# Kernel optimization log

Hardware: AMD Instinct MI355X
Metric: run time of the kernel (lower is better)

## Reference

```python
import jax, jax.numpy as jnp
import numpy as np

B, S, H = 2, 1024, 2048
NH, HD = 16, 128
L = 4  # num_prev_layers == attention_window


def _rope(x):
    # x: [..., S, D]; standard rotate-half RoPE, base 10000
    d = x.shape[-1]
    s = x.shape[-2]
    inv_freq = 1.0 / (10000.0 ** (jnp.arange(0, d, 2, dtype=jnp.float32) / d))
    freqs = jnp.outer(jnp.arange(s, dtype=jnp.float32), inv_freq)  # [S, d/2]
    cos, sin = jnp.cos(freqs), jnp.sin(freqs)
    x1, x2 = jnp.split(x, 2, axis=-1)
    return jnp.concatenate([x1 * cos - x2 * sin, x2 * cos + x1 * sin], axis=-1)


def setup_inputs() -> dict:
    key = jax.random.key(0)
    ks = jax.random.split(key, 8)
    std = 0.02
    return {
        "hidden_states": jax.random.normal(ks[0], (B, S, H), jnp.float32),
        "prev_hidden_states": jax.random.normal(ks[1], (L, B, S, H), jnp.float32),
        "Wq": jax.random.normal(ks[2], (H, NH * HD), jnp.float32) * std,
        "bq": jnp.zeros((NH * HD,), jnp.float32),
        "Wk": jax.random.normal(ks[3], (H, NH * HD), jnp.float32) * std,
        "bk": jnp.zeros((NH * HD,), jnp.float32),
        "Wv": jax.random.normal(ks[4], (H, NH * HD), jnp.float32) * std,
        "bv": jnp.zeros((NH * HD,), jnp.float32),
        "Wo": jax.random.normal(ks[5], (NH * HD, H), jnp.float32) * std,
        "bo": jnp.zeros((H,), jnp.float32),
        "Wg": jax.random.normal(ks[6], (H, L), jnp.float32) * std,
    }


def reference(hidden_states, prev_hidden_states, Wq, bq, Wk, bk, Wv, bv, Wo, bo, Wg):
    b, s, _ = hidden_states.shape
    # queries from current layer: [b, nh, s, hd], RoPE applied
    q = (hidden_states @ Wq + bq).reshape(b, s, NH, HD).transpose(0, 2, 1, 3)
    q = _rope(q)
    # keys/values from each prev layer: [L, b, nh, s, hd]
    k = (prev_hidden_states @ Wk + bk).reshape(L, b, s, NH, HD).transpose(0, 1, 3, 2, 4)
    k = _rope(k)
    v = (prev_hidden_states @ Wv + bv).reshape(L, b, s, NH, HD).transpose(0, 1, 3, 2, 4)
    # per-prev-layer attention (no mask)
    scores = jnp.einsum('bhqd,lbhkd->lbhqk', q, k) / jnp.sqrt(jnp.float32(HD))
    attn = jax.nn.softmax(scores, axis=-1)
    lo = jnp.einsum('lbhqk,lbhkd->lbhqd', attn, v)
    lo = lo.transpose(0, 1, 3, 2, 4).reshape(L, b, s, NH * HD)  # merge heads
    # softmax gate over pooled queries -> combine layer outputs
    layer_w = jax.nn.softmax(jnp.mean(hidden_states, axis=1) @ Wg, axis=-1)  # [b, L]
    out = jnp.einsum('lbsh,bl->bsh', lo, layer_w)
    return out @ Wo + bo
```

## Files before the change

### kernel.cpp

```cpp
#include <hip/hip_runtime.h>
#include <hip/hip_bf16.h>
#include <math.h>


typedef __bf16 bf16;
typedef __bf16 bf16x4v __attribute__((ext_vector_type(4)));
typedef __bf16 bf16x8 __attribute__((ext_vector_type(8)));
typedef float f32x4 __attribute__((ext_vector_type(4)));

#define DEV static __device__ __forceinline__

DEV void gload_lds16(const void* g, void* s) {
  __builtin_amdgcn_global_load_lds(
      (const __attribute__((address_space(1))) void*)g,
      (__attribute__((address_space(3))) void*)s, 16, 0, 0);
}

DEV f32x4 mfma16(bf16x8 a, bf16x8 b, f32x4 c) {
  return __builtin_amdgcn_mfma_f32_16x16x32_bf16(a, b, c, 0, 0, 0);
}

__global__ __launch_bounds__(256) void cvt_kernel(const float* __restrict__ in,
                                                  bf16* __restrict__ out, int n4) {
  int i = blockIdx.x * 256 + threadIdx.x;
  if (i >= n4) return;
  const float4 v = ((const float4*)in)[i];
  bf16x4v o;
  o.x = (bf16)v.x; o.y = (bf16)v.y; o.z = (bf16)v.z; o.w = (bf16)v.w;
  ((bf16x4v*)out)[i] = o;
}

__global__ __launch_bounds__(256) void twt_kernel(const float* __restrict__ W,
                                                  bf16* __restrict__ Wt) {
  __shared__ float tile[64][65];
  const int t = threadIdx.x;
  const int n0 = blockIdx.x * 64, k0 = blockIdx.y * 64;
#pragma unroll
  for (int ph = 0; ph < 16; ++ph) {
    int idx = ph * 256 + t, r = idx >> 6, c = idx & 63;
    tile[r][c] = W[(size_t)(k0 + r) * 2048 + n0 + c];
  }
  __syncthreads();
#pragma unroll
  for (int ph = 0; ph < 16; ++ph) {
    int idx = ph * 256 + t, r = idx >> 6, c = idx & 63;
    Wt[(size_t)(n0 + r) * 2048 + k0 + c] = (bf16)tile[c][r];
  }
}

__global__ __launch_bounds__(64) void rope_table_kernel(float* __restrict__ cosT,
                                                        float* __restrict__ sinT) {
  int s = blockIdx.x, j = threadIdx.x;
  float inv = powf(10000.0f, -(float)j * (1.0f / 64.0f));
  float a = (float)s * inv;
  cosT[s * 64 + j] = cosf(a);
  sinT[s * 64 + j] = sinf(a);
}

__global__ __launch_bounds__(256) void rope_kernel(const bf16* __restrict__ raw,
                                                   const float* __restrict__ cosT,
                                                   const float* __restrict__ sinT,
                                                   bf16* __restrict__ outp) {
  int rid = blockIdx.x * 16 + (threadIdx.x >> 4);
  int j = threadIdx.x & 15;
  int s = rid & 1023;
  const bf16* src = raw + (size_t)rid * 128 + 4 * j;
  bf16* dst = outp + (size_t)rid * 128 + 4 * j;
  bf16x4v x1 = *(const bf16x4v*)src;
  bf16x4v x2 = *(const bf16x4v*)(src + 64);
  f32x4 c = *(const f32x4*)(cosT + s * 64 + 4 * j);
  f32x4 sn = *(const f32x4*)(sinT + s * 64 + 4 * j);
  bf16x4v o1, o2;
#pragma unroll
  for (int k = 0; k < 4; ++k) {
    float a = (float)x1[k], b2 = (float)x2[k];
    o1[k] = (bf16)(a * c[k] - b2 * sn[k]);
    o2[k] = (bf16)(b2 * c[k] + a * sn[k]);
  }
  *(bf16x4v*)dst = o1;
  *(bf16x4v*)(dst + 64) = o2;
}

__global__ __launch_bounds__(256) void mean_part_kernel(const float* __restrict__ hs,
                                                        float* __restrict__ part) {
  int bc = blockIdx.x;
  int b = bc >> 3, c0 = (bc & 7) * 256;
  int ss = blockIdx.y;
  int col = c0 + threadIdx.x;
  float s = 0.f;
  for (int r = 0; r < 128; ++r)
    s += hs[((size_t)b * 1024 + ss * 128 + r) * 2048 + col];
  part[(size_t)ss * 4096 + b * 2048 + col] = s;
}

__global__ __launch_bounds__(256) void mean_fin_kernel(const float* __restrict__ part,
                                                       float* __restrict__ meanb) {
  int c = blockIdx.x * 256 + threadIdx.x;
  float s = 0.f;
#pragma unroll
  for (int j = 0; j < 8; ++j) s += part[(size_t)j * 4096 + c];
  meanb[c] = s * (1.0f / 1024.0f);
}

__global__ __launch_bounds__(256) void gate_kernel(const float* __restrict__ meanb,
                                                   const float* __restrict__ Wg,
                                                   float* __restrict__ lwout) {
  __shared__ float red[8][256];
  int t = threadIdx.x;
  float p[8];
#pragma unroll
  for (int j = 0; j < 8; ++j) p[j] = 0.f;
  for (int hh = t; hh < 2048; hh += 256) {
    float m0 = meanb[hh], m1 = meanb[2048 + hh];
#pragma unroll
    for (int ll = 0; ll < 4; ++ll) {
      float g = Wg[hh * 4 + ll];
      p[ll] += m0 * g;
      p[4 + ll] += m1 * g;
    }
  }
#pragma unroll
  for (int j = 0; j < 8; ++j) red[j][t] = p[j];
  __syncthreads();
  for (int s2 = 128; s2 > 0; s2 >>= 1) {
    if (t < s2) {
#pragma unroll
      for (int j = 0; j < 8; ++j) red[j][t] += red[j][t + s2];
    }
    __syncthreads();
  }
  if (t == 0) {
#pragma unroll
    for (int bb = 0; bb < 2; ++bb) {
      float v0 = red[bb * 4 + 0][0], v1 = red[bb * 4 + 1][0];
      float v2 = red[bb * 4 + 2][0], v3 = red[bb * 4 + 3][0];
      float mx = fmaxf(fmaxf(v0, v1), fmaxf(v2, v3));
      float e0 = __expf(v0 - mx), e1 = __expf(v1 - mx);
      float e2 = __expf(v2 - mx), e3 = __expf(v3 - mx);
      float inv = 1.0f / (e0 + e1 + e2 + e3);
      lwout[bb * 4 + 0] = e0 * inv;
      lwout[bb * 4 + 1] = e1 * inv;
      lwout[bb * 4 + 2] = e2 * inv;
      lwout[bb * 4 + 3] = e3 * inv;
    }
  }
}

template <int OUTMODE>
__global__ __launch_bounds__(256) void gemm_kernel(const bf16* __restrict__ A,
                                                   const bf16* __restrict__ Bt,
                                                   const float* __restrict__ bias,
                                                   void* __restrict__ Cout,
                                                   int M, int N, int K) {
  __shared__ __attribute__((aligned(16))) bf16 As[2][128 * 64];
  __shared__ __attribute__((aligned(16))) bf16 Bs[2][128 * 64];
  const int t = threadIdx.x;
  const int w = t >> 6, l = t & 63;
  const int lo = l & 15, hi = l >> 4;
  const int wr = w >> 1, wc = w & 1;

  const int nwg = gridDim.x * gridDim.y;
  int flat = blockIdx.y * gridDim.x + blockIdx.x;
  int swz = (flat & 7) * (nwg >> 3) + (flat >> 3);
  const int bx = swz % gridDim.x, by = swz / gridDim.x;

  f32x4 acc[4][4];
#pragma unroll
  for (int m = 0; m < 4; ++m)
#pragma unroll
    for (int n = 0; n < 4; ++n)
#pragma unroll
      for (int q = 0; q < 4; ++q) acc[m][n][q] = 0.f;

  int srow[4], scl[4];
#pragma unroll
  for (int p = 0; p < 4; ++p) {
    int id = p * 256 + t;
    int r = id >> 3, cph = id & 7;
    srow[p] = r;
    scl[p] = cph ^ (r & 7);
  }

  const bf16* Ab = A + (size_t)by * 128 * K;
  const bf16* Bb = Bt + (size_t)bx * 128 * K;

  auto stage = [&](int bi, int kt) {
#pragma unroll
    for (int p = 0; p < 4; ++p)
      gload_lds16(Ab + (size_t)srow[p] * K + kt + scl[p] * 8,
                  &As[bi][(p * 256 + w * 64) * 8]);
#pragma unroll
    for (int p = 0; p < 4; ++p)
      gload_lds16(Bb + (size_t)srow[p] * K + kt + scl[p] * 8,
                  &Bs[bi][(p * 256 + w * 64) * 8]);
  };

  stage(0, 0);
  int cur = 0;
  for (int kt = 0; kt < K; kt += 64) {
    if (kt + 64 < K) {
      stage(cur ^ 1, kt + 64);
      asm volatile("s_waitcnt vmcnt(8)" ::: "memory");
    } else {
      asm volatile("s_waitcnt vmcnt(0)" ::: "memory");
    }
    __builtin_amdgcn_s_barrier();
    __builtin_amdgcn_sched_barrier(0);
    __builtin_amdgcn_s_setprio(1);
#pragma unroll
    for (int ks = 0; ks < 2; ++ks) {
      bf16x8 af[4], bfr[4];
#pragma unroll
      for (int m = 0; m < 4; ++m) {
        int row = wr * 64 + m * 16 + lo;
        int ch = (ks * 4 + hi) ^ (row & 7);
        af[m] = *(const bf16x8*)&As[cur][row * 64 + ch * 8];
      }
#pragma unroll
      for (int n = 0; n < 4; ++n) {
        int row = wc * 64 + n * 16 + lo;
        int ch = (ks * 4 + hi) ^ (row & 7);
        bfr[n] = *(const bf16x8*)&Bs[cur][row * 64 + ch * 8];
      }
#pragma unroll
      for (int m = 0; m < 4; ++m)
#pragma unroll
        for (int n = 0; n < 4; ++n)
          acc[m][n] = mfma16(af[m], bfr[n], acc[m][n]);
    }
    __builtin_amdgcn_s_setprio(0);
    __builtin_amdgcn_s_barrier();
    cur ^= 1;
  }

#pragma unroll
  for (int n = 0; n < 4; ++n) {
    int col = bx * 128 + wc * 64 + n * 16 + lo;
    float bb = bias[col];
#pragma unroll
    for (int m = 0; m < 4; ++m) {
#pragma unroll
      for (int i = 0; i < 4; ++i) {
        size_t row = (size_t)by * 128 + wr * 64 + m * 16 + hi * 4 + i;
        float v = acc[m][n][i] + bb;
        if (OUTMODE == 1)
          ((float*)Cout)[row * N + col] = v;
        else if (OUTMODE == 0)
          ((bf16*)Cout)[row * N + col] = (bf16)v;
        else {
          size_t g = (row >> 10) * 16 + (col >> 7);
          ((bf16*)Cout)[(g * 1024 + (row & 1023)) * 128 + (col & 127)] = (bf16)v;
        }
      }
    }
  }
}

__global__ __launch_bounds__(512, 2) void gemm_kv_kernel(
    const bf16* __restrict__ prev, const bf16* __restrict__ WkT,
    const bf16* __restrict__ WvT, const float* __restrict__ bk,
    const float* __restrict__ bv, bf16* __restrict__ Kout,
    bf16* __restrict__ Vout) {
  __shared__ __attribute__((aligned(16))) bf16 As[2][16384];
  __shared__ __attribute__((aligned(16))) bf16 Bs[2][16384];
  const int t = threadIdx.x;
  const int w = t >> 6, l = t & 63;
  const int lo = l & 15, hi = l >> 4;
  const int wm = w >> 2, wn = w & 3;

  const int bid = blockIdx.x;
  const int grp = bid >> 8;
  const int sub = bid & 255;
  const int swz = (sub & 7) * 32 + (sub >> 3);
  const int mt = (grp == 0) ? (swz >> 3) : (swz & 7);
  const int nt = (grp == 0) ? (swz & 7) : (swz >> 3);
  const bf16* Ab = ((grp == 0) ? prev : WvT) + (size_t)mt * 256 * 2048;
  const bf16* Bb = ((grp == 0) ? WkT : prev) + (size_t)nt * 256 * 2048;

  const int r0 = t >> 2;
  const int c8 = ((t & 3) ^ ((r0 >> 1) & 3)) * 8;

  f32x4 acc[8][4];
#pragma unroll
  for (int m = 0; m < 8; ++m)
#pragma unroll
    for (int n = 0; n < 4; ++n)
#pragma unroll
      for (int q = 0; q < 4; ++q) acc[m][n][q] = 0.f;

  auto gA = [&](int bi, int kh, int p, int koff) {
    gload_lds16(Ab + (size_t)(p * 128 + r0) * 2048 + koff + kh * 32 + c8,
                &As[bi][kh * 8192 + p * 4096 + w * 512]);
  };
  auto gB = [&](int bi, int kh, int p, int koff) {
    gload_lds16(Bb + (size_t)(p * 128 + r0) * 2048 + koff + kh * 32 + c8,
                &Bs[bi][kh * 8192 + p * 4096 + w * 512]);
  };

  gA(0, 0, 0, 0); gA(0, 0, 1, 0);
  gB(0, 0, 0, 0); gB(0, 0, 1, 0);
  gA(0, 1, 0, 0); gA(0, 1, 1, 0);
  gB(0, 1, 0, 0); gB(0, 1, 1, 0);
  asm volatile("s_waitcnt vmcnt(4)" ::: "memory");
  __builtin_amdgcn_s_barrier();

  int cur = 0;
  for (int kt = 0; kt < 32; ++kt) {
    const int nxt = cur ^ 1;
    const int koff = (kt + 1) * 64;
    const bool pf = kt < 31;
    bf16x8 af[8], bfr[2];

#pragma unroll
    for (int m = 0; m < 8; ++m) {
      int row = wm * 128 + m * 16 + lo;
      int slot = hi ^ ((row >> 1) & 3);
      af[m] = *(const bf16x8*)&As[cur][row * 32 + slot * 8];
    }
#pragma unroll
    for (int n = 0; n < 2; ++n) {
      int row = wn * 64 + n * 16 + lo;
      int slot = hi ^ ((row >> 1) & 3);
      bfr[n] = *(const bf16x8*)&Bs[cur][row * 32 + slot * 8];
    }
    if (pf) { gA(nxt, 0, 0, koff); gA(nxt, 0, 1, koff); }
    __builtin_amdgcn_s_barrier();
    __builtin_amdgcn_s_setprio(1);
#pragma unroll
    for (int m = 0; m < 8; ++m) {
      acc[m][0] = mfma16(af[m], bfr[0], acc[m][0]);
      acc[m][1] = mfma16(af[m], bfr[1], acc[m][1]);
    }
    __builtin_amdgcn_s_setprio(0);
    __builtin_amdgcn_s_barrier();

#pragma unroll
    for (int n = 0; n < 2; ++n) {
      int row = wn * 64 + (n + 2) * 16 + lo;
      int slot = hi ^ ((row >> 1) & 3);
      bfr[n] = *(const bf16x8*)&Bs[cur][row * 32 + slot * 8];
    }
    if (pf) {
      gB(nxt, 0, 0, koff); gB(nxt, 0, 1, koff);
      asm volatile("s_waitcnt vmcnt(4)" ::: "memory");
    } else {
      asm volatile("s_waitcnt vmcnt(0)" ::: "memory");
    }
    __builtin_amdgcn_s_barrier();
    __builtin_amdgcn_s_setprio(1);
#pragma unroll
    for (int m = 0; m < 8; ++m) {
      acc[m][2] = mfma16(af[m], bfr[0], acc[m][2]);
      acc[m][3] = mfma16(af[m], bfr[1], acc[m][3]);
    }
    __builtin_amdgcn_s_setprio(0);
    __builtin_amdgcn_s_barrier();

#pragma unroll
    for (int m = 0; m < 8; ++m) {
      int row = wm * 128 + m * 16 + lo;
      int slot = hi ^ ((row >> 1) & 3);
      af[m] = *(const bf16x8*)&As[cur][8192 + row * 32 + slot * 8];
    }
#pragma unroll
    for (int n = 0; n < 2; ++n) {
      int row = wn * 64 + n * 16 + lo;
      int slot = hi ^ ((row >> 1) & 3);
      bfr[n] = *(const bf16x8*)&Bs[cur][8192 + row * 32 + slot * 8];
    }
    if (pf) { gA(nxt, 1, 0, koff); gA(nxt, 1, 1, koff); }
    __builtin_amdgcn_s_barrier();
    __builtin_amdgcn_s_setprio(1);
#pragma unroll
    for (int m = 0; m < 8; ++m) {
      acc[m][0] = mfma16(af[m], bfr[0], acc[m][0]);
      acc[m][1] = mfma16(af[m], bfr[1], acc[m][1]);
    }
    __builtin_amdgcn_s_setprio(0);
    __builtin_amdgcn_s_barrier();

#pragma unroll
    for (int n = 0; n < 2; ++n) {
      int row = wn * 64 + (n + 2) * 16 + lo;
      int slot = hi ^ ((row >> 1) & 3);
      bfr[n] = *(const bf16x8*)&Bs[cur][8192 + row * 32 + slot * 8];
    }
    if (pf) {
      gB(nxt, 1, 0, koff); gB(nxt, 1, 1, koff);
      asm volatile("s_waitcnt vmcnt(4)" ::: "memory");
    } else {
      asm volatile("s_waitcnt vmcnt(0)" ::: "memory");
    }
    __builtin_amdgcn_s_barrier();
    __builtin_amdgcn_s_setprio(1);
#pragma unroll
    for (int m = 0; m < 8; ++m) {
      acc[m][2] = mfma16(af[m], bfr[0], acc[m][2]);
      acc[m][3] = mfma16(af[m], bfr[1], acc[m][3]);
    }
    __builtin_amdgcn_s_setprio(0);
    __builtin_amdgcn_s_barrier();

    cur = nxt;
  }

  if (grp == 0) {
#pragma unroll
    for (int n = 0; n < 4; ++n) {
      int col = nt * 256 + wn * 64 + n * 16 + lo;
      float bb = bk[col];
#pragma unroll
      for (int m = 0; m < 8; ++m) {
#pragma unroll
        for (int i = 0; i < 4; ++i) {
          size_t row = (size_t)mt * 256 + wm * 128 + m * 16 + hi * 4 + i;
          float v = acc[m][n][i] + bb;
          size_t g = (row >> 10) * 16 + (col >> 7);
          Kout[(g * 1024 + (row & 1023)) * 128 + (col & 127)] = (bf16)v;
        }
      }
    }
  } else {
#pragma unroll
    for (int m = 0; m < 8; ++m) {
#pragma unroll
      for (int i = 0; i < 4; ++i) {
        size_t row = (size_t)mt * 256 + wm * 128 + m * 16 + hi * 4 + i;
        float rb = bv[row];
#pragma unroll
        for (int n = 0; n < 4; ++n) {
          int col = nt * 256 + wn * 64 + n * 16 + lo;
          int pos64 = ((n >> 1) << 5) + ((lo >> 2) << 3) + ((n & 1) << 2) + (lo & 3);
          int colp = (col & ~63) | pos64;
          float v = acc[m][n][i] + rb;
          Vout[(size_t)(colp >> 10) * 2097152 + row * 1024 + (colp & 1023)] =
              (bf16)v;
        }
      }
    }
  }
}

__global__ __launch_bounds__(256, 2) void attn_kernel(const bf16* __restrict__ Q,
                                                      const bf16* __restrict__ Kb,
                                                      const bf16* __restrict__ Vt,
                                                      const float* __restrict__ lw,
                                                      bf16* __restrict__ Obuf) {
  __shared__ __attribute__((aligned(16))) bf16 Ks[2][64 * 128];
  __shared__ __attribute__((aligned(16))) bf16 Vs[2][128 * 64];
  const int t = threadIdx.x, w = t >> 6, l = t & 63;
  const int lo = l & 15, hi = l >> 4;
  const int bh = blockIdx.x;
  const int qt = blockIdx.y;
  const int li = blockIdx.z;
  const int b = bh >> 4, h = bh & 15;
  const float C2 = 0.08838834764831845f * 1.44269504f;
  const float M2 = 64.0f * C2;

  bf16x8 qf[2][4];
#pragma unroll
  for (int qs = 0; qs < 2; ++qs) {
    const bf16* qptr =
        Q + ((size_t)bh * 1024 + qt * 128 + w * 32 + qs * 16 + lo) * 128;
#pragma unroll
    for (int db = 0; db < 4; ++db)
      qf[qs][db] = *(const bf16x8*)(qptr + db * 32 + hi * 8);
  }

  int krow[4], kcl[4], vrow[4], vcl[4];
#pragma unroll
  for (int p = 0; p < 4; ++p) {
    int id = p * 256 + t;
    krow[p] = id >> 4;
    kcl[p] = (id & 15) ^ (krow[p] & 7);
    vrow[p] = id >> 3;
    vcl[p] = (id & 7) ^ (vrow[p] & 7);
  }

  const bf16* Kl = Kb + ((size_t)li * 32 + bh) * (size_t)131072;
  const bf16* Vl = Vt + ((size_t)li * 32 + bh) * (size_t)131072;

  float si0 = 0.f, si1 = 0.f;
  f32x4 oacc[2][8];
#pragma unroll
  for (int qs = 0; qs < 2; ++qs)
#pragma unroll
    for (int dc = 0; dc < 8; ++dc)
#pragma unroll
      for (int q = 0; q < 4; ++q) oacc[qs][dc][q] = 0.f;

  auto stage = [&](int bi, int kt2) {
    const bf16* Ksrc = Kl + (size_t)kt2 * 8192;
#pragma unroll
    for (int p = 0; p < 4; ++p)
      gload_lds16(Ksrc + (size_t)krow[p] * 128 + kcl[p] * 8,
                  &Ks[bi][(p * 256 + w * 64) * 8]);
#pragma unroll
    for (int p = 0; p < 4; ++p)
      gload_lds16(Vl + (size_t)vrow[p] * 1024 + kt2 * 64 + vcl[p] * 8,
                  &Vs[bi][(p * 256 + w * 64) * 8]);
  };

  auto softmax_step = [&](f32x4 (&sa)[4], float& si, bf16x8 (&pf2)[2]) {
    float rs = 0.f;
    bf16x4v pk[4];
#pragma unroll
    for (int kc = 0; kc < 4; ++kc) {
#pragma unroll
      for (int i = 0; i < 4; ++i) {
        float pf_ = __builtin_amdgcn_exp2f(fmaf(sa[kc][i], C2, -M2));
        rs += pf_;
        pk[kc][i] = (bf16)pf_;
      }
    }
    rs += __shfl_xor(rs, 16);
    rs += __shfl_xor(rs, 32);
    si += rs;
    pf2[0] = __builtin_shufflevector(pk[0], pk[1], 0, 1, 2, 3, 4, 5, 6, 7);
    pf2[1] = __builtin_shufflevector(pk[2], pk[3], 0, 1, 2, 3, 4, 5, 6, 7);
  };

  stage(0, 0);
  int cur = 0;
  for (int kt = 0; kt < 16; ++kt) {
    if (kt < 15) {
      stage(cur ^ 1, kt + 1);
      asm volatile("s_waitcnt vmcnt(8)" ::: "memory");
    } else {
      asm volatile("s_waitcnt vmcnt(0)" ::: "memory");
    }
    __builtin_amdgcn_s_barrier();
    __builtin_amdgcn_sched_barrier(0);

    f32x4 sa[2][4];
#pragma unroll
    for (int qs = 0; qs < 2; ++qs)
#pragma unroll
      for (int kc = 0; kc < 4; ++kc)
#pragma unroll
        for (int q = 0; q < 4; ++q) sa[qs][kc][q] = 0.f;
    __builtin_amdgcn_s_setprio(1);
#pragma unroll
    for (int kc = 0; kc < 4; ++kc) {
      int row = kc * 16 + lo;
#pragma unroll
      for (int db = 0; db < 4; ++db) {
        int ch = (db * 4 + hi) ^ (row & 7);
        bf16x8 kf = *(const bf16x8*)&Ks[cur][row * 128 + ch * 8];
        sa[0][kc] = mfma16(kf, qf[0][db], sa[0][kc]);
        sa[1][kc] = mfma16(kf, qf[1][db], sa[1][kc]);
      }
    }
    __builtin_amdgcn_s_setprio(0);

    bf16x8 pfr[2][2];
    softmax_step(sa[0], si0, pfr[0]);
    softmax_step(sa[1], si1, pfr[1]);

    __builtin_amdgcn_s_setprio(1);
#pragma unroll
    for (int kvc = 0; kvc < 2; ++kvc) {
#pragma unroll
      for (int dc = 0; dc < 8; ++dc) {
        int rowv = dc * 16 + lo;
        int ch = (kvc * 4 + hi) ^ (rowv & 7);
        bf16x8 vf = *(const bf16x8*)&Vs[cur][rowv * 64 + ch * 8];
        oacc[0][dc] = mfma16(pfr[0][kvc], vf, oacc[0][dc]);
        oacc[1][dc] = mfma16(pfr[1][kvc], vf, oacc[1][dc]);
      }
    }
    __builtin_amdgcn_s_setprio(0);
    __builtin_amdgcn_s_barrier();
    cur ^= 1;
  }

  float wl = lw[b * 4 + li];
#pragma unroll
  for (int qs = 0; qs < 2; ++qs) {
    float sv = (qs == 0) ? si0 : si1;
    float inv[4];
#pragma unroll
    for (int i = 0; i < 4; ++i) inv[i] = wl / __shfl(sv, hi * 4 + i);
#pragma unroll
    for (int dc = 0; dc < 8; ++dc) {
      int col = h * 128 + dc * 16 + lo;
#pragma unroll
      for (int i = 0; i < 4; ++i) {
        int srow = qt * 128 + w * 32 + qs * 16 + hi * 4 + i;
        Obuf[((size_t)(li * 2 + b) * 1024 + srow) * 2048 + col] =
            (bf16)(oacc[qs][dc][i] * inv[i]);
      }
    }
  }
}

__global__ __launch_bounds__(256) void comb_kernel(const bf16* __restrict__ Obuf,
                                                   bf16* __restrict__ comb) {
  size_t i = ((size_t)blockIdx.x * 256 + threadIdx.x) * 8;
  bf16x8 a0 = *(const bf16x8*)(Obuf + i);
  bf16x8 a1 = *(const bf16x8*)(Obuf + 4194304 + i);
  bf16x8 a2 = *(const bf16x8*)(Obuf + 8388608 + i);
  bf16x8 a3 = *(const bf16x8*)(Obuf + 12582912 + i);
  bf16x8 o;
#pragma unroll
  for (int j = 0; j < 8; ++j)
    o[j] = (bf16)((float)a0[j] + (float)a1[j] + (float)a2[j] + (float)a3[j]);
  *(bf16x8*)(comb + i) = o;
}

extern "C" void kernel_launch(void* const* d_in, const int* in_sizes, int n_in,
                              void* d_out, int out_size, void* d_ws, size_t ws_size,
                              hipStream_t stream) {
  (void)in_sizes; (void)n_in; (void)out_size; (void)ws_size;
  const float* hs = (const float*)d_in[0];
  const float* prev = (const float*)d_in[1];
  const float* Wq = (const float*)d_in[2];
  const float* bq = (const float*)d_in[3];
  const float* Wk = (const float*)d_in[4];
  const float* bk = (const float*)d_in[5];
  const float* Wv = (const float*)d_in[6];
  const float* bv = (const float*)d_in[7];
  const float* Wo = (const float*)d_in[8];
  const float* bo = (const float*)d_in[9];
  const float* Wg = (const float*)d_in[10];
  float* out = (float*)d_out;

  char* ws = (char*)d_ws;
  bf16* hs_bf = (bf16*)(ws + 0);
  bf16* prev_bf = (bf16*)(ws + 8388608);
  bf16* WqT = (bf16*)(ws + 41943040);
  bf16* WkT = (bf16*)(ws + 50331648);
  bf16* WvT = (bf16*)(ws + 58720256);
  bf16* Qraw2 = (bf16*)(ws + 67108864);
  bf16* WoT = (bf16*)(ws + 75497472);
  bf16* Kraw2 = (bf16*)(ws + 83886080);
  bf16* Vt = (bf16*)(ws + 117440512);
  float* cosT = (float*)(ws + 150994944);
  float* sinT = (float*)(ws + 151257088);
  float* part = (float*)(ws + 151519232);
  float* meanb = (float*)(ws + 151650304);
  float* lwbuf = (float*)(ws + 151666688);
  bf16* Qbf = hs_bf;
  bf16* Kbf = prev_bf;
  bf16* Obuf = Kraw2;
  bf16* comb = (bf16*)(ws + 0);

  cvt_kernel<<<4096, 256, 0, stream>>>(hs, hs_bf, 2048 * 2048 / 4);
  cvt_kernel<<<16384, 256, 0, stream>>>(prev, prev_bf, 8192 * 2048 / 4);

  twt_kernel<<<dim3(32, 32), 256, 0, stream>>>(Wq, WqT);
  twt_kernel<<<dim3(32, 32), 256, 0, stream>>>(Wk, WkT);
  twt_kernel<<<dim3(32, 32), 256, 0, stream>>>(Wv, WvT);
  twt_kernel<<<dim3(32, 32), 256, 0, stream>>>(Wo, WoT);

  rope_table_kernel<<<1024, 64, 0, stream>>>(cosT, sinT);
  mean_part_kernel<<<dim3(16, 8), 256, 0, stream>>>(hs, part);
  mean_fin_kernel<<<16, 256, 0, stream>>>(part, meanb);
  gate_kernel<<<1, 256, 0, stream>>>(meanb, Wg, lwbuf);

  gemm_kernel<3><<<dim3(16, 16), 256, 0, stream>>>(hs_bf, WqT, bq, Qraw2, 2048, 2048, 2048);
  gemm_kv_kernel<<<512, 512, 0, stream>>>(prev_bf, WkT, WvT, bk, bv, Kraw2, Vt);

  rope_kernel<<<2048, 256, 0, stream>>>(Qraw2, cosT, sinT, Qbf);
  rope_kernel<<<8192, 256, 0, stream>>>(Kraw2, cosT, sinT, Kbf);

  attn_kernel<<<dim3(32, 8, 4), 256, 0, stream>>>(Qbf, Kbf, Vt, lwbuf, Obuf);

  comb_kernel<<<2048, 256, 0, stream>>>(Obuf, comb);

  gemm_kernel<1><<<dim3(16, 16), 256, 0, stream>>>(comb, WoT, bo, out, 2048, 2048, 2048);
}
```

Before: 362.8 us.

## Fuse K RoPE into KV GEMM epilogue with LDS-staged coalesced stores

The KV projection GEMM epilogue now stages each 128-row half of the output tile in shared memory. It then applies RoPE to K directly from that staged copy and writes vectorized, coalesced rows. V's permuted transposed layout is also written with 16-byte stores. This removes the separate K RoPE kernel and its full read/write pass over the K buffer, at the cost of extra barriers and LDS traffic in the epilogue.

```diff
diff --git a/kernel.cpp b/kernel.cpp
--- a/kernel.cpp
+++ b/kernel.cpp
@@ -259,10 +259,12 @@
 __global__ __launch_bounds__(512, 2) void gemm_kv_kernel(
     const bf16* __restrict__ prev, const bf16* __restrict__ WkT,
     const bf16* __restrict__ WvT, const float* __restrict__ bk,
-    const float* __restrict__ bv, bf16* __restrict__ Kout,
+    const float* __restrict__ bv, const float* __restrict__ cosT,
+    const float* __restrict__ sinT, bf16* __restrict__ Kout,
     bf16* __restrict__ Vout) {
-  __shared__ __attribute__((aligned(16))) bf16 As[2][16384];
-  __shared__ __attribute__((aligned(16))) bf16 Bs[2][16384];
+  __shared__ __attribute__((aligned(16))) bf16 SH[65536];
+  bf16* AsP0 = SH;
+  bf16* BsP0 = SH + 32768;
   const int t = threadIdx.x;
   const int w = t >> 6, l = t & 63;
   const int lo = l & 15, hi = l >> 4;
@@ -290,11 +292,11 @@
 
   auto gA = [&](int bi, int kh, int p, int koff) {
     gload_lds16(Ab + (size_t)(p * 128 + r0) * 2048 + koff + kh * 32 + c8,
-                &As[bi][kh * 8192 + p * 4096 + w * 512]);
+                &AsP0[bi * 16384 + kh * 8192 + p * 4096 + w * 512]);
   };
   auto gB = [&](int bi, int kh, int p, int koff) {
     gload_lds16(Bb + (size_t)(p * 128 + r0) * 2048 + koff + kh * 32 + c8,
-                &Bs[bi][kh * 8192 + p * 4096 + w * 512]);
+                &BsP0[bi * 16384 + kh * 8192 + p * 4096 + w * 512]);
   };
 
   gA(0, 0, 0, 0); gA(0, 0, 1, 0);
@@ -310,18 +312,20 @@
     const int koff = (kt + 1) * 64;
     const bool pf = kt < 31;
     bf16x8 af[8], bfr[2];
+    const bf16* Acur = AsP0 + cur * 16384;
+    const bf16* Bcur = BsP0 + cur * 16384;
 
 #pragma unroll
     for (int m = 0; m < 8; ++m) {
       int row = wm * 128 + m * 16 + lo;
       int slot = hi ^ ((row >> 1) & 3);
-      af[m] = *(const bf16x8*)&As[cur][row * 32 + slot * 8];
+      af[m] = *(const bf16x8*)&Acur[row * 32 + slot * 8];
     }
 #pragma unroll
     for (int n = 0; n < 2; ++n) {
       int row = wn * 64 + n * 16 + lo;
       int slot = hi ^ ((row >> 1) & 3);
-      bfr[n] = *(const bf16x8*)&Bs[cur][row * 32 + slot * 8];
+      bfr[n] = *(const bf16x8*)&Bcur[row * 32 + slot * 8];
     }
     if (pf) { gA(nxt, 0, 0, koff); gA(nxt, 0, 1, koff); }
     __builtin_amdgcn_s_barrier();
@@ -338,7 +342,7 @@
     for (int n = 0; n < 2; ++n) {
       int row = wn * 64 + (n + 2) * 16 + lo;
       int slot = hi ^ ((row >> 1) & 3);
-      bfr[n] = *(const bf16x8*)&Bs[cur][row * 32 + slot * 8];
+      bfr[n] = *(const bf16x8*)&Bcur[row * 32 + slot * 8];
     }
     if (pf) {
       gB(nxt, 0, 0, koff); gB(nxt, 0, 1, koff);
@@ -360,13 +364,13 @@
     for (int m = 0; m < 8; ++m) {
       int row = wm * 128 + m * 16 + lo;
       int slot = hi ^ ((row >> 1) & 3);
-      af[m] = *(const bf16x8*)&As[cur][8192 + row * 32 + slot * 8];
+      af[m] = *(const bf16x8*)&Acur[8192 + row * 32 + slot * 8];
     }
 #pragma unroll
     for (int n = 0; n < 2; ++n) {
       int row = wn * 64 + n * 16 + lo;
       int slot = hi ^ ((row >> 1) & 3);
-      bfr[n] = *(const bf16x8*)&Bs[cur][8192 + row * 32 + slot * 8];
+      bfr[n] = *(const bf16x8*)&Bcur[8192 + row * 32 + slot * 8];
     }
     if (pf) { gA(nxt, 1, 0, koff); gA(nxt, 1, 1, koff); }
     __builtin_amdgcn_s_barrier();
@@ -383,7 +387,7 @@
     for (int n = 0; n < 2; ++n) {
       int row = wn * 64 + (n + 2) * 16 + lo;
       int slot = hi ^ ((row >> 1) & 3);
-      bfr[n] = *(const bf16x8*)&Bs[cur][8192 + row * 32 + slot * 8];
+      bfr[n] = *(const bf16x8*)&Bcur[8192 + row * 32 + slot * 8];
     }
     if (pf) {
       gB(nxt, 1, 0, koff); gB(nxt, 1, 1, koff);
@@ -404,40 +408,66 @@
     cur = nxt;
   }
 
-  if (grp == 0) {
-#pragma unroll
-    for (int n = 0; n < 4; ++n) {
-      int col = nt * 256 + wn * 64 + n * 16 + lo;
-      float bb = bk[col];
+#pragma unroll
+  for (int p = 0; p < 2; ++p) {
+    if (wm == p) {
 #pragma unroll
       for (int m = 0; m < 8; ++m) {
 #pragma unroll
         for (int i = 0; i < 4; ++i) {
-          size_t row = (size_t)mt * 256 + wm * 128 + m * 16 + hi * 4 + i;
-          float v = acc[m][n][i] + bb;
-          size_t g = (row >> 10) * 16 + (col >> 7);
-          Kout[(g * 1024 + (row & 1023)) * 128 + (col & 127)] = (bf16)v;
+          int rowl = m * 16 + hi * 4 + i;
+          float rb = (grp == 1) ? bv[(size_t)mt * 256 + p * 128 + rowl] : 0.f;
+#pragma unroll
+          for (int n = 0; n < 4; ++n) {
+            int coll = wn * 64 + n * 16 + lo;
+            float bb = (grp == 0) ? bk[nt * 256 + coll] : rb;
+            SH[rowl * 264 + coll] = (bf16)(acc[m][n][i] + bb);
+          }
         }
       }
     }
-  } else {
-#pragma unroll
-    for (int m = 0; m < 8; ++m) {
-#pragma unroll
-      for (int i = 0; i < 4; ++i) {
-        size_t row = (size_t)mt * 256 + wm * 128 + m * 16 + hi * 4 + i;
-        float rb = bv[row];
-#pragma unroll
-        for (int n = 0; n < 4; ++n) {
-          int col = nt * 256 + wn * 64 + n * 16 + lo;
-          int pos64 = ((n >> 1) << 5) + ((lo >> 2) << 3) + ((n & 1) << 2) + (lo & 3);
-          int colp = (col & ~63) | pos64;
-          float v = acc[m][n][i] + rb;
-          Vout[(size_t)(colp >> 10) * 2097152 + row * 1024 + (colp & 1023)] =
-              (bf16)v;
+    __builtin_amdgcn_s_barrier();
+
+    if (grp == 0) {
+      int tokl = t >> 2, head = (t >> 1) & 1, half = t & 1;
+      size_t grow = (size_t)mt * 256 + p * 128 + tokl;
+      int s_idx = (int)(grow & 1023);
+      size_t gg = (grow >> 10) * 16 + nt * 2 + head;
+      const bf16* x1p = &SH[tokl * 264 + head * 128];
+      const bf16* x2p = x1p + 64;
+      bf16* dst = Kout + (gg * 1024 + s_idx) * 128 + half * 64;
+      const float* cp = cosT + s_idx * 64;
+      const float* sp = sinT + s_idx * 64;
+#pragma unroll
+      for (int cb = 0; cb < 8; ++cb) {
+        bf16x8 x1 = *(const bf16x8*)(x1p + cb * 8);
+        bf16x8 x2 = *(const bf16x8*)(x2p + cb * 8);
+        bf16x8 o;
+#pragma unroll
+        for (int k = 0; k < 8; ++k) {
+          float cc = cp[cb * 8 + k], ss = sp[cb * 8 + k];
+          float a = (float)x1[k], b2 = (float)x2[k];
+          o[k] = (bf16)(half ? (b2 * cc + a * ss) : (a * cc - b2 * ss));
         }
-      }
-    }
+        *(bf16x8*)(dst + cb * 8) = o;
+      }
+    } else {
+      int featl = t >> 2, q = t & 3;
+      size_t feat_g = (size_t)mt * 256 + p * 128 + featl;
+      int tokbase = nt * 256 + q * 64;
+      bf16* dst = Vout + (size_t)(tokbase >> 10) * 2097152 + feat_g * 1024 +
+                  (tokbase & 1023);
+      const bf16* src = &SH[featl * 264 + q * 64];
+#pragma unroll
+      for (int o16 = 0; o16 < 8; ++o16) {
+        int tb = (o16 >> 2) * 32 + (o16 & 3) * 4;
+        bf16x4v lo4 = *(const bf16x4v*)(src + tb);
+        bf16x4v hi4 = *(const bf16x4v*)(src + tb + 16);
+        bf16x8 o = __builtin_shufflevector(lo4, hi4, 0, 1, 2, 3, 4, 5, 6, 7);
+        *(bf16x8*)(dst + o16 * 8) = o;
+      }
+    }
+    __builtin_amdgcn_s_barrier();
   }
 }
 
@@ -633,7 +663,7 @@
   bf16* WvT = (bf16*)(ws + 58720256);
   bf16* Qraw2 = (bf16*)(ws + 67108864);
   bf16* WoT = (bf16*)(ws + 75497472);
-  bf16* Kraw2 = (bf16*)(ws + 83886080);
+  bf16* Kbf = (bf16*)(ws + 83886080);
   bf16* Vt = (bf16*)(ws + 117440512);
   float* cosT = (float*)(ws + 150994944);
   float* sinT = (float*)(ws + 151257088);
@@ -641,8 +671,7 @@
   float* meanb = (float*)(ws + 151650304);
   float* lwbuf = (float*)(ws + 151666688);
   bf16* Qbf = hs_bf;
-  bf16* Kbf = prev_bf;
-  bf16* Obuf = Kraw2;
+  bf16* Obuf = prev_bf;
   bf16* comb = (bf16*)(ws + 0);
 
   cvt_kernel<<<4096, 256, 0, stream>>>(hs, hs_bf, 2048 * 2048 / 4);
@@ -659,10 +688,10 @@
   gate_kernel<<<1, 256, 0, stream>>>(meanb, Wg, lwbuf);
 
   gemm_kernel<3><<<dim3(16, 16), 256, 0, stream>>>(hs_bf, WqT, bq, Qraw2, 2048, 2048, 2048);
-  gemm_kv_kernel<<<512, 512, 0, stream>>>(prev_bf, WkT, WvT, bk, bv, Kraw2, Vt);
+  gemm_kv_kernel<<<512, 512, 0, stream>>>(prev_bf, WkT, WvT, bk, bv, cosT, sinT,
+                                          Kbf, Vt);
 
   rope_kernel<<<2048, 256, 0, stream>>>(Qraw2, cosT, sinT, Qbf);
-  rope_kernel<<<8192, 256, 0, stream>>>(Kraw2, cosT, sinT, Kbf);
 
   attn_kernel<<<dim3(32, 8, 4), 256, 0, stream>>>(Qbf, Kbf, Vt, lwbuf, Obuf);
 
```

Measured after the change: 377.2 us. +3.9%, slower.
